# Optimization experiments

Hardware: AMD Instinct MI355X
Metric: run time of the kernel (lower is better)

## Reference

```python
import jax, jax.numpy as jnp
import numpy as np
from jax import lax
from jax.scipy.special import logsumexp

KX = jnp.array([[1., 0., -1.], [2., 0., -2.], [1., 0., -1.]], jnp.float32).reshape(1, 1, 3, 3)
KY = jnp.array([[1., 2., 1.], [0., 0., 0.], [-1., -2., -1.]], jnp.float32).reshape(1, 1, 3, 3)
SINK_EPS = 0.05 ** 2  # geomloss SamplesLoss('sinkhorn', p=2, blur=0.05): eps = blur**p
SINK_ITERS = 10
N_SUB = 4096


def _gauss1d(size, sigma):
    x = jnp.arange(size, dtype=jnp.float32) - (size - 1) / 2.0
    k = jnp.exp(-(x * x) / (2.0 * sigma * sigma))
    return k / k.sum()


def _sep_filter(x, k, sym_pad):
    # separable 2D filter; x [B,C,H,W], k [ks]. VALID conv; optional symmetric pad (scipy 'reflect').
    B, C, H, W = x.shape
    xr = x.reshape(B * C, 1, H, W)
    if sym_pad:
        r = k.shape[0] // 2
        xr = jnp.pad(xr, ((0, 0), (0, 0), (r, r), (r, r)), mode='symmetric')
    o = lax.conv_general_dilated(xr, k.reshape(1, 1, -1, 1), (1, 1), 'VALID')
    o = lax.conv_general_dilated(o, k.reshape(1, 1, 1, -1), (1, 1), 'VALID')
    return o.reshape(B, C, o.shape[2], o.shape[3])


def _ssim_per_sample(x, y):
    # standard gaussian-window SSIM (11x11, sigma=1.5, data_range=1.0), mean per sample -> [B]
    k = _gauss1d(11, 1.5)
    mu1, mu2 = _sep_filter(x, k, False), _sep_filter(y, k, False)
    s11 = _sep_filter(x * x, k, False) - mu1 * mu1
    s22 = _sep_filter(y * y, k, False) - mu2 * mu2
    s12 = _sep_filter(x * y, k, False) - mu1 * mu2
    C1, C2 = 0.01 ** 2, 0.03 ** 2
    m = ((2 * mu1 * mu2 + C1) * (2 * s12 + C2)) / ((mu1 * mu1 + mu2 * mu2 + C1) * (s11 + s22 + C2))
    return m.mean(axis=(1, 2, 3))


def _sobel(x):
    # SobelGrad.forward: per-channel magnitude, per-(b,c) max-normalized, channel-mean -> [B,1,H,W]
    B, C, H, W = x.shape
    xr = x.reshape(B * C, 1, H, W)
    gx = lax.conv_general_dilated(xr, KX, (1, 1), ((1, 1), (1, 1)))
    gy = lax.conv_general_dilated(xr, KY, (1, 1), ((1, 1), (1, 1)))
    mag = jnp.sqrt(gx * gx + gy * gy + 1e-6).reshape(B, C, H, W)
    mag = mag / jnp.maximum(mag.max(axis=(2, 3), keepdims=True), 1e-6)
    return mag.mean(1, keepdims=True)


def _avgpool2(x):
    B, C, H, W = x.shape
    return x.reshape(B, C, H // 2, 2, W // 2, 2).mean(axis=(3, 5))


def _charb_mean(d):
    return jnp.sqrt(d * d + 1e-6).mean()  # charbonnier eps=1e-3


def _ot_eps(x, y):
    # entropic OT value with uniform weights, log-domain Sinkhorn, envelope gradient (geomloss-style:
    # iterations detached, one differentiable update at the end).
    N, M = x.shape[0], y.shape[0]
    C = 0.5 * (jnp.sum(x * x, 1)[:, None] + jnp.sum(y * y, 1)[None, :] - 2.0 * x @ y.T)  # p=2 cost |x-y|^2/2
    Cd = lax.stop_gradient(C)
    loga, logb = -float(np.log(N)), -float(np.log(M))
    def body(carry, _):
        f, g = carry
        g = -SINK_EPS * logsumexp(loga + (f[:, None] - Cd) / SINK_EPS, axis=0)
        f = -SINK_EPS * logsumexp(logb + (g[None, :] - Cd) / SINK_EPS, axis=1)
        return (f, g), None
    (f, g), _ = lax.scan(body, (jnp.zeros((N,), x.dtype), jnp.zeros((M,), x.dtype)), None, length=SINK_ITERS)
    f = lax.stop_gradient(f)
    g = -SINK_EPS * logsumexp(loga + (f[:, None] - C) / SINK_EPS, axis=0)
    f = -SINK_EPS * logsumexp(logb + (g[None, :] - C) / SINK_EPS, axis=1)
    return f.mean() + g.mean()


def _sinkhorn_div(x, y):
    return _ot_eps(x, y) - 0.5 * _ot_eps(x, x) - 0.5 * _ot_eps(y, y)


def _forward(y, mri, pet, mask, ehat, idx):
    B, C, H, W = y.shape
    y_gray = y.mean(1, keepdims=True)
    ssim_m = 1.0 - _ssim_per_sample(y_gray, mri).mean()
    ssim_p = 1.0 - _ssim_per_sample(y, pet).mean()
    g_cons = (_charb_mean(_sobel(y_gray) - _sobel(mri))
              + _charb_mean(_sobel(_avgpool2(y).mean(1, keepdims=True)) - _sobel(_avgpool2(mri))))
    aux = jnp.abs(ehat - lax.stop_gradient(_sobel(mri))).mean()
    # per-sample masked point clouds, fixed 4096-point subsample (idx ~ randperm[:4096])
    y_pts = (y * mask).reshape(B, C, H * W).transpose(0, 2, 1)    # [B,HW,3]
    pet_pts = (pet * mask).reshape(B, C, H * W).transpose(0, 2, 1)
    y_s = jnp.take_along_axis(y_pts, idx[..., None], axis=1)      # [B,4096,3]
    pet_s = jnp.take_along_axis(pet_pts, idx[..., None], axis=1)
    include = ((mask.reshape(B, -1) > 0.1).sum(1) >= 32).astype(y.dtype)  # 'continue' guard
    L_transport = (include * jax.vmap(_sinkhorn_div)(y_s, pet_s)).sum() / B
    L_out = (include * ((y * (1.0 - mask)) ** 2).mean(axis=(1, 2, 3))).sum() / B
    mri_rgb = jnp.broadcast_to(mri, y.shape)
    L_ssim = (include * (1.0 - _ssim_per_sample(y * mask, mri_rgb * mask))).sum() / B
    loss_transport = 0.8 * L_transport + 0.3 * L_out + 0.5 * L_ssim  # alpha, beta, gamma
    L_intensity = 2.5 * jnp.mean((y * mask - pet * mask) ** 2)
    # gaussian_smooth: scipy gaussian_filter sigma=1, truncate=4 -> radius 4, mode 'reflect';
    # torch path detaches before smoothing -> stop_gradient
    smoothed = lax.stop_gradient(_sep_filter(y, _gauss1d(9, 1.0), True))
    L_smooth = jnp.mean((smoothed - y) ** 2)
    total = loss_transport + L_intensity + 0.2 * L_smooth
    return total, ssim_m, ssim_p, g_cons, aux


def setup_inputs() -> dict:
    key = jax.random.key(0)
    ks = jax.random.split(key, 5)
    B, C, H, W = 2, 3, 256, 256
    y = jax.random.uniform(ks[0], (B, C, H, W), jnp.float32)
    mri = jax.random.uniform(ks[1], (B, 1, H, W), jnp.float32)
    pet = jax.random.uniform(ks[2], (B, C, H, W), jnp.float32)
    mask = jax.random.uniform(ks[3], (B, 1, H, W), jnp.float32)
    ehat = jax.random.uniform(ks[4], (B, 1, H, W), jnp.float32)
    rng = np.random.default_rng(0)
    idx = jnp.asarray(np.stack([rng.permutation(H * W)[:N_SUB] for _ in range(B)]), dtype=jnp.int32)
    return {"y": y, "mri": mri, "pet": pet, "mask": mask, "ehat": ehat, "idx": idx}


def reference(y, mri, pet, mask, ehat, idx):
    return _forward(y, mri, pet, mask, ehat, idx)
```

## Files before the change

### kernel.cpp

```cpp
#include <hip/hip_runtime.h>
#include <math.h>

#define INV_EPS_L2E 577.0780163555854f
#define EPS_LOGN 0.02079441542f
#define EPS_LN2 0.00173286795f

#define NPTS 4096
#define CHUNK 64
#define NCH 64
#define CPT 8
#define COLS_PER_BLK 2048
#define NCB 2
#define QSTRIDE (NCH * NPTS)

typedef float v2f __attribute__((ext_vector_type(2)));

constexpr int A_SSIMA  = 0;
constexpr int A_SSIMB  = 2;
constexpr int A_SSIMC  = 4;
constexpr int A_CH1    = 6;
constexpr int A_CH2    = 7;
constexpr int A_AUX    = 8;
constexpr int A_INT    = 9;
constexpr int A_LOUT   = 10;
constexpr int A_CNT    = 12;
constexpr int A_SMOOTH = 14;
constexpr int A_SINK   = 16;
constexpr int A_MAX    = 32;

__device__ __forceinline__ float blockSum(float v, int tid) {
#pragma unroll
    for (int o = 32; o; o >>= 1) v += __shfl_down(v, o, 64);
    __shared__ float sh[4];
    __syncthreads();
    if ((tid & 63) == 0) sh[tid >> 6] = v;
    __syncthreads();
    return sh[0] + sh[1] + sh[2] + sh[3];
}

__device__ __forceinline__ float blockMax(float v, int tid) {
#pragma unroll
    for (int o = 32; o; o >>= 1) v = fmaxf(v, __shfl_down(v, o, 64));
    __shared__ float sh[4];
    __syncthreads();
    if ((tid & 63) == 0) sh[tid >> 6] = v;
    __syncthreads();
    return fmaxf(fmaxf(sh[0], sh[1]), fmaxf(sh[2], sh[3]));
}

__global__ __launch_bounds__(256) void egf_prep(const float* __restrict__ y,
                                                const float* __restrict__ pet,
                                                const float* __restrict__ mask,
                                                float* __restrict__ ygray,
                                                float* __restrict__ acc) {
    int b = blockIdx.y;
    int p = blockIdx.x * 256 + threadIdx.x;
    float m  = mask[b * 65536 + p];
    float y0 = y[(b * 3 + 0) * 65536 + p];
    float y1 = y[(b * 3 + 1) * 65536 + p];
    float y2 = y[(b * 3 + 2) * 65536 + p];
    float q0 = pet[(b * 3 + 0) * 65536 + p];
    float q1 = pet[(b * 3 + 1) * 65536 + p];
    float q2 = pet[(b * 3 + 2) * 65536 + p];
    ygray[b * 65536 + p] = (y0 + y1 + y2) * (1.0f / 3.0f);
    float d0 = m * y0 - m * q0, d1 = m * y1 - m * q1, d2 = m * y2 - m * q2;
    float inten = d0 * d0 + d1 * d1 + d2 * d2;
    float im = 1.0f - m;
    float o0 = y0 * im, o1 = y1 * im, o2 = y2 * im;
    float lout = o0 * o0 + o1 * o1 + o2 * o2;
    float cnt = (m > 0.1f) ? 1.0f : 0.0f;
    float t;
    t = blockSum(inten, threadIdx.x); if (threadIdx.x == 0) atomicAdd(&acc[A_INT], t);
    t = blockSum(lout,  threadIdx.x); if (threadIdx.x == 0) atomicAdd(&acc[A_LOUT + b], t);
    t = blockSum(cnt,   threadIdx.x); if (threadIdx.x == 0) atomicAdd(&acc[A_CNT + b], t);
}

__global__ __launch_bounds__(256) void egf_pool(const float* __restrict__ y,
                                                const float* __restrict__ mri,
                                                float* __restrict__ py,
                                                float* __restrict__ pmri) {
    int b = blockIdx.y;
    int po = blockIdx.x * 256 + threadIdx.x;
    int i = po >> 7, j = po & 127;
    int p0 = (i * 2) * 256 + j * 2;
    float s = 0.0f;
#pragma unroll
    for (int c = 0; c < 3; c++) {
        const float* ip = y + (b * 3 + c) * 65536;
        s += ip[p0] + ip[p0 + 1] + ip[p0 + 256] + ip[p0 + 257];
    }
    py[b * 16384 + po] = s * (1.0f / 12.0f);
    const float* mp = mri + b * 65536;
    pmri[b * 16384 + po] = (mp[p0] + mp[p0 + 1] + mp[p0 + 256] + mp[p0 + 257]) * 0.25f;
}

__global__ __launch_bounds__(256) void egf_sobel(const float* __restrict__ in,
                                                 float* __restrict__ mag,
                                                 unsigned* __restrict__ mx,
                                                 int H, int logH) {
    int b = blockIdx.y;
    int p = blockIdx.x * 256 + threadIdx.x;
    int HH = H * H;
    const float* ip = in + b * HH;
    int i = p >> logH, j = p & (H - 1);
    auto at = [&](int ii, int jj) -> float {
        return (ii >= 0 && ii < H && jj >= 0 && jj < H) ? ip[(ii << logH) + jj] : 0.0f;
    };
    float a00 = at(i - 1, j - 1), a01 = at(i - 1, j), a02 = at(i - 1, j + 1);
    float a10 = at(i, j - 1),                         a12 = at(i, j + 1);
    float a20 = at(i + 1, j - 1), a21 = at(i + 1, j), a22 = at(i + 1, j + 1);
    float gx = a00 - a02 + 2.0f * a10 - 2.0f * a12 + a20 - a22;
    float gy = a00 + 2.0f * a01 + a02 - a20 - 2.0f * a21 - a22;
    float m = sqrtf(gx * gx + gy * gy + 1e-6f);
    mag[b * HH + p] = m;
    float bm = blockMax(m, threadIdx.x);
    if (threadIdx.x == 0) atomicMax(mx + b, __float_as_uint(bm));
}

__global__ __launch_bounds__(256) void egf_charb(const float* __restrict__ magA,
                                                 const float* __restrict__ magB,
                                                 const unsigned* __restrict__ mxA,
                                                 const unsigned* __restrict__ mxB,
                                                 const float* __restrict__ ehat,
                                                 float* __restrict__ accC,
                                                 float* __restrict__ accAux,
                                                 int HH) {
    int b = blockIdx.y;
    int p = blockIdx.x * 256 + threadIdx.x;
    float c = 0.0f, au = 0.0f;
    float da = fmaxf(__uint_as_float(mxA[b]), 1e-6f);
    float db = fmaxf(__uint_as_float(mxB[b]), 1e-6f);
    if (p < HH) {
        float sa = magA[b * HH + p] / da;
        float sb = magB[b * HH + p] / db;
        float d = sa - sb;
        c = sqrtf(d * d + 1e-6f);
        if (ehat) au = fabsf(ehat[b * HH + p] - sb);
    }
    float tc = blockSum(c, threadIdx.x);
    if (threadIdx.x == 0) atomicAdd(accC, tc);
    if (ehat) {
        float ta = blockSum(au, threadIdx.x);
        if (threadIdx.x == 0) atomicAdd(accAux, ta);
    }
}

__global__ __launch_bounds__(256) void egf_ssim(const float* __restrict__ X, int xBS, int xCS,
                                                const float* __restrict__ Y, int yBS, int yCS,
                                                const float* __restrict__ M,
                                                int C_, float* __restrict__ accB) {
    int bc = blockIdx.z; int b = bc / C_; int c = bc - b * C_;
    const float* xp = X + b * xBS + c * xCS;
    const float* yp = Y + b * yBS + c * yCS;
    const float* mp = M ? (M + b * 65536) : nullptr;
    __shared__ float sx[26][27];
    __shared__ float sy[26][27];
    int ti = blockIdx.x * 16, tj = blockIdx.y * 16;
    int tid = threadIdx.y * 16 + threadIdx.x;
    for (int t = tid; t < 26 * 26; t += 256) {
        int li = t / 26, lj = t - li * 26;
        int gi = ti + li, gj = tj + lj;
        float a = 0.0f, bb = 0.0f;
        if (gi < 256 && gj < 256) {
            int p = (gi << 8) + gj;
            float m = mp ? mp[p] : 1.0f;
            a = xp[p] * m; bb = yp[p] * m;
        }
        sx[li][lj] = a; sy[li][lj] = bb;
    }
    __syncthreads();
    float w[11];
    {
        float s = 0.0f;
#pragma unroll
        for (int i = 0; i < 11; i++) { float d = (float)(i - 5); w[i] = expf(-d * d * (1.0f / 4.5f)); s += w[i]; }
        float inv = 1.0f / s;
#pragma unroll
        for (int i = 0; i < 11; i++) w[i] *= inv;
    }
    int oi = ti + threadIdx.y, oj = tj + threadIdx.x;
    float val = 0.0f;
    if (oi < 246 && oj < 246) {
        float mu1 = 0, mu2 = 0, xx = 0, yy = 0, xy = 0;
        for (int di = 0; di < 11; di++) {
            float wi = w[di];
#pragma unroll
            for (int dj = 0; dj < 11; dj++) {
                float ww = wi * w[dj];
                float a  = sx[threadIdx.y + di][threadIdx.x + dj];
                float bb = sy[threadIdx.y + di][threadIdx.x + dj];
                mu1 += ww * a; mu2 += ww * bb;
                xx += ww * a * a; yy += ww * bb * bb; xy += ww * a * bb;
            }
        }
        float s11 = xx - mu1 * mu1, s22 = yy - mu2 * mu2, s12 = xy - mu1 * mu2;
        const float C1 = 1e-4f, C2 = 9e-4f;
        val = ((2.0f * mu1 * mu2 + C1) * (2.0f * s12 + C2)) /
              ((mu1 * mu1 + mu2 * mu2 + C1) * (s11 + s22 + C2));
    }
    float tot = blockSum(val, tid);
    if (tid == 0) atomicAdd(&accB[b], tot);
}

__device__ __forceinline__ int refl256(int i) { return i < 0 ? -1 - i : (i > 255 ? 511 - i : i); }

__device__ __forceinline__ void gauss9(float* w) {
    float s = 0.0f;
#pragma unroll
    for (int t = 0; t < 9; t++) { float d = (float)(t - 4); w[t] = expf(-0.5f * d * d); s += w[t]; }
    float inv = 1.0f / s;
#pragma unroll
    for (int t = 0; t < 9; t++) w[t] *= inv;
}

__global__ __launch_bounds__(256) void egf_smoothV(const float* __restrict__ y, float* __restrict__ tmp) {
    int g = blockIdx.x * 256 + threadIdx.x;
    int bc = g >> 16; int p = g & 65535; int i = p >> 8, j = p & 255;
    float w[9]; gauss9(w);
    const float* ip = y + bc * 65536;
    float s = 0.0f;
#pragma unroll
    for (int t = 0; t < 9; t++) s += w[t] * ip[(refl256(i + t - 4) << 8) + j];
    tmp[g] = s;
}

__global__ __launch_bounds__(256) void egf_smoothH(const float* __restrict__ tmp,
                                                   const float* __restrict__ y,
                                                   float* __restrict__ acc) {
    int g = blockIdx.x * 256 + threadIdx.x;
    int bc = g >> 16; int p = g & 65535; int i = p >> 8, j = p & 255;
    float w[9]; gauss9(w);
    const float* tp = tmp + bc * 65536;
    float s = 0.0f;
#pragma unroll
    for (int t = 0; t < 9; t++) s += w[t] * tp[(i << 8) + refl256(j + t - 4)];
    float d = s - y[g];
    float tt = blockSum(d * d, threadIdx.x);
    if (threadIdx.x == 0) atomicAdd(acc, tt);
}

__global__ __launch_bounds__(256) void egf_gather(const float* __restrict__ y,
                                                  const float* __restrict__ pet,
                                                  const float* __restrict__ mask,
                                                  const int* __restrict__ idx,
                                                  float4* __restrict__ pts) {
    int t = blockIdx.x * 256 + threadIdx.x;
    int b = t >> 12, j = t & 4095;
    int p = idx[b * 4096 + j];
    float m = mask[b * 65536 + p];
    float a0 = y[(b * 3 + 0) * 65536 + p] * m;
    float a1 = y[(b * 3 + 1) * 65536 + p] * m;
    float a2 = y[(b * 3 + 2) * 65536 + p] * m;
    pts[(b * 2 + 0) * 4096 + j] = make_float4(a0, a1, a2, 0.5f * (a0 * a0 + a1 * a1 + a2 * a2));
    float c0 = pet[(b * 3 + 0) * 65536 + p] * m;
    float c1 = pet[(b * 3 + 1) * 65536 + p] * m;
    float c2 = pet[(b * 3 + 2) * 65536 + p] * m;
    pts[(b * 2 + 1) * 4096 + j] = make_float4(c0, c1, c2, 0.5f * (c0 * c0 + c1 * c1 + c2 * c2));
}

__device__ __forceinline__ float stageCombine(const float* __restrict__ Pin_m,
                                              const float* __restrict__ Pin_s,
                                              int qbase, int row, int h, int r_local,
                                              float* sm, float* ss, int tid) {
    const float* pm = Pin_m + qbase + h * 16 * NPTS + row;
    const float* ps = Pin_s + qbase + h * 16 * NPTS + row;
    float mv[16], sv[16];
#pragma unroll
    for (int k = 0; k < 16; k++) mv[k] = pm[k * NPTS];
#pragma unroll
    for (int k = 0; k < 16; k++) sv[k] = ps[k * NPTS];
    float m16 = -3.4e38f;
#pragma unroll
    for (int k = 0; k < 16; k++) m16 = fmaxf(m16, mv[k]);
    float s16 = 0.0f;
#pragma unroll
    for (int k = 0; k < 16; k++) s16 += sv[k] * __builtin_amdgcn_exp2f(mv[k] - m16);
    sm[h * 64 + r_local] = m16;
    ss[h * 64 + r_local] = s16;
    __syncthreads();
    float v = 0.0f;
    if (tid < 64) {
        float m0 = sm[tid], m1 = sm[64 + tid], m2 = sm[128 + tid], m3 = sm[192 + tid];
        float M = fmaxf(fmaxf(m0, m1), fmaxf(m2, m3));
        float S = ss[tid]       * __builtin_amdgcn_exp2f(m0 - M) +
                  ss[64 + tid]  * __builtin_amdgcn_exp2f(m1 - M) +
                  ss[128 + tid] * __builtin_amdgcn_exp2f(m2 - M) +
                  ss[192 + tid] * __builtin_amdgcn_exp2f(m3 - M);
        v = EPS_LOGN - EPS_LN2 * (M + log2f(S));
    }
    return v;
}

__global__ __launch_bounds__(256) void egf_sink_half5(const float4* __restrict__ pts,
                                                      const float* __restrict__ Pin_m,
                                                      const float* __restrict__ Pin_s,
                                                      float* __restrict__ Pout_m,
                                                      float* __restrict__ Pout_s,
                                                      int dir, int init) {
    int q = blockIdx.z; int b = q / 3, t = q - b * 3;
    int xsel = (t == 2) ? 1 : 0;
    int ysel = (t == 1) ? 0 : 1;
    int rsel = (dir == 0) ? xsel : ysel;
    int csel = (dir == 0) ? ysel : xsel;
    const float4* rowP = pts + (b * 2 + rsel) * NPTS;
    const float4* colP = pts + (b * 2 + csel) * NPTS;

    __shared__ float4 srow[CHUNK];
    __shared__ float sm[256], ss[256];
    int tid = threadIdx.x;
    int chunk = blockIdx.y;
    int r_local = tid & 63, h = tid >> 6;
    int row = chunk * CHUNK + r_local;

    float v = 0.0f;
    if (!init)
        v = stageCombine(Pin_m, Pin_s, q * QSTRIDE, row, h, r_local, sm, ss, tid);
    if (tid < 64) {
        float4 pp = rowP[row];
        srow[tid] = make_float4(pp.x * INV_EPS_L2E, pp.y * INV_EPS_L2E,
                                pp.z * INV_EPS_L2E, (v - pp.w) * INV_EPS_L2E);
    }
    __syncthreads();

    int col0 = blockIdx.x * COLS_PER_BLK + tid;
    v2f cx[4], cy[4], cz[4], cw[4];
#pragma unroll
    for (int p = 0; p < 4; p++) {
        float4 c0 = colP[col0 + (2 * p) * 256];
        float4 c1 = colP[col0 + (2 * p + 1) * 256];
        cx[p] = (v2f){c0.x, c1.x};
        cy[p] = (v2f){c0.y, c1.y};
        cz[p] = (v2f){c0.z, c1.z};
        cw[p] = (v2f){c0.w * INV_EPS_L2E, c1.w * INV_EPS_L2E};
    }
    v2f mx[4];
#pragma unroll
    for (int p = 0; p < 4; p++) mx[p] = -3.4e38f;
#pragma unroll 4
    for (int r = 0; r < CHUNK; r++) {
        float4 rp = srow[r];
        v2f rx = rp.x, ry = rp.y, rz = rp.z, rw = rp.w;
#pragma unroll
        for (int p = 0; p < 4; p++) {
            v2f e = rw;
            e = __builtin_elementwise_fma(rx, cx[p], e);
            e = __builtin_elementwise_fma(ry, cy[p], e);
            e = __builtin_elementwise_fma(rz, cz[p], e);
            mx[p] = __builtin_elementwise_max(mx[p], e);
        }
    }
    v2f sa[4];
#pragma unroll
    for (int p = 0; p < 4; p++) sa[p] = 0.0f;
#pragma unroll 4
    for (int r = 0; r < CHUNK; r++) {
        float4 rp = srow[r];
        v2f rx = rp.x, ry = rp.y, rz = rp.z, rw = rp.w;
#pragma unroll
        for (int p = 0; p < 4; p++) {
            v2f e = rw - mx[p];
            e = __builtin_elementwise_fma(rx, cx[p], e);
            e = __builtin_elementwise_fma(ry, cy[p], e);
            e = __builtin_elementwise_fma(rz, cz[p], e);
            v2f ex;
            ex.x = __builtin_amdgcn_exp2f(e.x);
            ex.y = __builtin_amdgcn_exp2f(e.y);
            sa[p] += ex;
        }
    }
    float* om = Pout_m + q * QSTRIDE + chunk * NPTS;
    float* os = Pout_s + q * QSTRIDE + chunk * NPTS;
#pragma unroll
    for (int p = 0; p < 4; p++) {
        v2f mstore = mx[p] - cw[p];
        om[col0 + (2 * p) * 256]     = mstore.x;
        om[col0 + (2 * p + 1) * 256] = mstore.y;
        os[col0 + (2 * p) * 256]     = sa[p].x;
        os[col0 + (2 * p + 1) * 256] = sa[p].y;
    }
}

__global__ __launch_bounds__(256) void egf_sink_val5(const float* __restrict__ Pf_m,
                                                     const float* __restrict__ Pf_s,
                                                     const float* __restrict__ Pg_m,
                                                     const float* __restrict__ Pg_s,
                                                     float* __restrict__ acc) {
    int q = blockIdx.y;
    int side = blockIdx.x >> 6;
    int chunk = blockIdx.x & 63;
    const float* Pm = side ? Pg_m : Pf_m;
    const float* Ps = side ? Pg_s : Pf_s;
    __shared__ float sm[256], ss[256];
    int tid = threadIdx.x;
    int r_local = tid & 63, h = tid >> 6;
    int row = chunk * CHUNK + r_local;
    float v = stageCombine(Pm, Ps, q * QSTRIDE, row, h, r_local, sm, ss, tid);
    float tot = blockSum(v, tid);
    if (tid == 0) atomicAdd(&acc[A_SINK + q], tot * (1.0f / 4096.0f));
}

__global__ void egf_finalize(const float* __restrict__ acc, float* __restrict__ out) {
    if (threadIdx.x != 0 || blockIdx.x != 0) return;
    const float AREA = 246.0f * 246.0f;
    float ssim_m = 1.0f - (acc[A_SSIMA] + acc[A_SSIMA + 1]) / (2.0f * AREA);
    float ssim_p = 1.0f - (acc[A_SSIMB] + acc[A_SSIMB + 1]) / (2.0f * 3.0f * AREA);
    float g_cons = acc[A_CH1] / (2.0f * 65536.0f) + acc[A_CH2] / (2.0f * 16384.0f);
    float aux = acc[A_AUX] / (2.0f * 65536.0f);
    float inc0 = (acc[A_CNT]     >= 31.5f) ? 1.0f : 0.0f;
    float inc1 = (acc[A_CNT + 1] >= 31.5f) ? 1.0f : 0.0f;
    const float* v = acc + A_SINK;
    float Lt = (inc0 * (v[0] - 0.5f * v[1] - 0.5f * v[2]) +
                inc1 * (v[3] - 0.5f * v[4] - 0.5f * v[5])) * 0.5f;
    float Lo = (inc0 * acc[A_LOUT] + inc1 * acc[A_LOUT + 1]) / (3.0f * 65536.0f) * 0.5f;
    float Ls = (inc0 * (1.0f - acc[A_SSIMC] / (3.0f * AREA)) +
                inc1 * (1.0f - acc[A_SSIMC + 1] / (3.0f * AREA))) * 0.5f;
    float Li = 2.5f * acc[A_INT] / (2.0f * 3.0f * 65536.0f);
    float Lsm = acc[A_SMOOTH] / (2.0f * 3.0f * 65536.0f);
    float total = 0.8f * Lt + 0.3f * Lo + 0.5f * Ls + Li + 0.2f * Lsm;
    out[0] = total; out[1] = ssim_m; out[2] = ssim_p; out[3] = g_cons; out[4] = aux;
}

extern "C" void kernel_launch(void* const* d_in, const int* in_sizes, int n_in,
                              void* d_out, int out_size, void* d_ws, size_t ws_size,
                              hipStream_t stream) {
    const float* y    = (const float*)d_in[0];
    const float* mri  = (const float*)d_in[1];
    const float* pet  = (const float*)d_in[2];
    const float* mask = (const float*)d_in[3];
    const float* ehat = (const float*)d_in[4];
    const int*   idx  = (const int*)d_in[5];
    float* out = (float*)d_out;
    float* ws  = (float*)d_ws;

    float* acc   = ws;
    float4* pts  = (float4*)(ws + 64);
    float* base  = ws + 64 + 65536;

    float* Pf_m = base;
    float* Pf_s = base + QSTRIDE * 6;
    float* Pg_m = base + 2 * QSTRIDE * 6;
    float* Pg_s = base + 3 * QSTRIDE * 6;
    float* ibase = base + 4 * QSTRIDE * 6;

    float* ygray    = ibase;
    float* py       = ygray + 131072;
    float* pmri     = py + 32768;
    float* mag_yg   = pmri + 32768;
    float* mag_mri  = mag_yg + 131072;
    float* mag_py   = mag_mri + 131072;
    float* mag_pmri = mag_py + 32768;
    float* tmp      = mag_pmri + 32768;

    hipMemsetAsync(acc, 0, 64 * sizeof(float), stream);

    unsigned* mx = (unsigned*)(acc + A_MAX);

    egf_prep<<<dim3(256, 2), 256, 0, stream>>>(y, pet, mask, ygray, acc);
    egf_pool<<<dim3(64, 2), 256, 0, stream>>>(y, mri, py, pmri);
    egf_sobel<<<dim3(256, 2), 256, 0, stream>>>(ygray, mag_yg, mx + 0, 256, 8);
    egf_sobel<<<dim3(256, 2), 256, 0, stream>>>(mri, mag_mri, mx + 2, 256, 8);
    egf_sobel<<<dim3(64, 2), 256, 0, stream>>>(py, mag_py, mx + 4, 128, 7);
    egf_sobel<<<dim3(64, 2), 256, 0, stream>>>(pmri, mag_pmri, mx + 6, 128, 7);
    egf_charb<<<dim3(256, 2), 256, 0, stream>>>(mag_yg, mag_mri, mx + 0, mx + 2, ehat,
                                                acc + A_CH1, acc + A_AUX, 65536);
    egf_charb<<<dim3(64, 2), 256, 0, stream>>>(mag_py, mag_pmri, mx + 4, mx + 6, nullptr,
                                               acc + A_CH2, nullptr, 16384);
    egf_ssim<<<dim3(16, 16, 2), dim3(16, 16), 0, stream>>>(ygray, 65536, 0, mri, 65536, 0,
                                                           nullptr, 1, acc + A_SSIMA);
    egf_ssim<<<dim3(16, 16, 6), dim3(16, 16), 0, stream>>>(y, 196608, 65536, pet, 196608, 65536,
                                                           nullptr, 3, acc + A_SSIMB);
    egf_ssim<<<dim3(16, 16, 6), dim3(16, 16), 0, stream>>>(y, 196608, 65536, mri, 65536, 0,
                                                           mask, 3, acc + A_SSIMC);
    egf_smoothV<<<1536, 256, 0, stream>>>(y, tmp);
    egf_smoothH<<<1536, 256, 0, stream>>>(tmp, y, acc + A_SMOOTH);
    egf_gather<<<32, 256, 0, stream>>>(y, pet, mask, idx, pts);

    dim3 sgrid(NCB, NCH, 6);
    for (int it = 0; it < 11; ++it) {
        egf_sink_half5<<<sgrid, 256, 0, stream>>>(pts, Pf_m, Pf_s, Pg_m, Pg_s, 0, it == 0 ? 1 : 0);
        egf_sink_half5<<<sgrid, 256, 0, stream>>>(pts, Pg_m, Pg_s, Pf_m, Pf_s, 1, 0);
    }
    egf_sink_val5<<<dim3(128, 6), 256, 0, stream>>>(Pf_m, Pf_s, Pg_m, Pg_s, acc);
    egf_finalize<<<1, 64, 0, stream>>>(acc, out);
}
```

Before: 874.0 us.

## Fuse Sinkhorn half-iterations into one persistent cooperative kernel with grid sync

Replaces the 22 separate Sinkhorn half-step launches with a single cooperative persistent kernel. Blocks loop over the 768 tiles and use grid-wide syncs between half-iterations. The aim is to remove per-launch overhead and the drain/refill gaps between the small kernels. In exchange, grid.sync adds its own cost, and if the grid is smaller than the tile count some blocks process tiles serially. A fallback to the old launch loop runs if the cooperative launch fails.

New measurement: 2.066 ms. 2.36x slower.

```diff
diff --git a/kernel.cpp b/kernel.cpp
--- a/kernel.cpp
+++ b/kernel.cpp
@@ -1,5 +1,8 @@
 #include <hip/hip_runtime.h>
+#include <hip/hip_cooperative_groups.h>
 #include <math.h>
+
+namespace cg = cooperative_groups;
 
 #define INV_EPS_L2E 577.0780163555854f
 #define EPS_LOGN 0.02079441542f
@@ -11,6 +14,7 @@
 #define CPT 8
 #define COLS_PER_BLK 2048
 #define NCB 2
+#define NTILES 768
 #define QSTRIDE (NCH * NPTS)
 
 typedef float v2f __attribute__((ext_vector_type(2)));
@@ -291,26 +295,25 @@
     return v;
 }
 
-__global__ __launch_bounds__(256) void egf_sink_half5(const float4* __restrict__ pts,
-                                                      const float* __restrict__ Pin_m,
-                                                      const float* __restrict__ Pin_s,
-                                                      float* __restrict__ Pout_m,
-                                                      float* __restrict__ Pout_s,
-                                                      int dir, int init) {
-    int q = blockIdx.z; int b = q / 3, t = q - b * 3;
+__device__ __forceinline__ void sinkTileBody(const float4* __restrict__ pts,
+                                             const float* __restrict__ Pin_m,
+                                             const float* __restrict__ Pin_s,
+                                             float* __restrict__ Pout_m,
+                                             float* __restrict__ Pout_s,
+                                             int dir, int init, int tile,
+                                             float4* srow, float* sm, float* ss, int tid) {
+    int q = tile >> 7;
+    int r = tile & 127;
+    int chunk = r >> 1;
+    int cb = r & 1;
+    int b = q / 3, t = q - b * 3;
     int xsel = (t == 2) ? 1 : 0;
     int ysel = (t == 1) ? 0 : 1;
-    int rsel = (dir == 0) ? xsel : ysel;
-    int csel = (dir == 0) ? ysel : xsel;
-    const float4* rowP = pts + (b * 2 + rsel) * NPTS;
-    const float4* colP = pts + (b * 2 + csel) * NPTS;
-
-    __shared__ float4 srow[CHUNK];
-    __shared__ float sm[256], ss[256];
-    int tid = threadIdx.x;
-    int chunk = blockIdx.y;
+    const float4* rowP = pts + (b * 2 + (dir ? ysel : xsel)) * NPTS;
+    const float4* colP = pts + (b * 2 + (dir ? xsel : ysel)) * NPTS;
     int r_local = tid & 63, h = tid >> 6;
     int row = chunk * CHUNK + r_local;
+    int col0 = cb * COLS_PER_BLK + tid;
 
     float v = 0.0f;
     if (!init)
@@ -322,7 +325,6 @@
     }
     __syncthreads();
 
-    int col0 = blockIdx.x * COLS_PER_BLK + tid;
     v2f cx[4], cy[4], cz[4], cw[4];
 #pragma unroll
     for (int p = 0; p < 4; p++) {
@@ -337,8 +339,8 @@
 #pragma unroll
     for (int p = 0; p < 4; p++) mx[p] = -3.4e38f;
 #pragma unroll 4
-    for (int r = 0; r < CHUNK; r++) {
-        float4 rp = srow[r];
+    for (int rr = 0; rr < CHUNK; rr++) {
+        float4 rp = srow[rr];
         v2f rx = rp.x, ry = rp.y, rz = rp.z, rw = rp.w;
 #pragma unroll
         for (int p = 0; p < 4; p++) {
@@ -353,8 +355,8 @@
 #pragma unroll
     for (int p = 0; p < 4; p++) sa[p] = 0.0f;
 #pragma unroll 4
-    for (int r = 0; r < CHUNK; r++) {
-        float4 rp = srow[r];
+    for (int rr = 0; rr < CHUNK; rr++) {
+        float4 rp = srow[rr];
         v2f rx = rp.x, ry = rp.y, rz = rp.z, rw = rp.w;
 #pragma unroll
         for (int p = 0; p < 4; p++) {
@@ -378,6 +380,45 @@
         os[col0 + (2 * p) * 256]     = sa[p].x;
         os[col0 + (2 * p + 1) * 256] = sa[p].y;
     }
+    __syncthreads();
+}
+
+__global__ __launch_bounds__(256, 3) void egf_sink_coop(const float4* __restrict__ pts,
+                                                        float* __restrict__ Pf_m,
+                                                        float* __restrict__ Pf_s,
+                                                        float* __restrict__ Pg_m,
+                                                        float* __restrict__ Pg_s,
+                                                        int ntiles) {
+    cg::grid_group grid = cg::this_grid();
+    __shared__ float4 srow[CHUNK];
+    __shared__ float sm[256], ss[256];
+    int tid = threadIdx.x;
+    int nb = gridDim.x;
+
+    for (int hh = 0; hh < 22; hh++) {
+        int dir = hh & 1;
+        const float* Pin_m = dir ? Pg_m : Pf_m;
+        const float* Pin_s = dir ? Pg_s : Pf_s;
+        float* Pout_m = dir ? Pf_m : Pg_m;
+        float* Pout_s = dir ? Pf_s : Pg_s;
+        for (int tile = blockIdx.x; tile < ntiles; tile += nb)
+            sinkTileBody(pts, Pin_m, Pin_s, Pout_m, Pout_s, dir, hh == 0, tile,
+                         srow, sm, ss, tid);
+        if (hh < 21) grid.sync();
+    }
+}
+
+__global__ __launch_bounds__(256) void egf_sink_half5(const float4* __restrict__ pts,
+                                                      const float* __restrict__ Pin_m,
+                                                      const float* __restrict__ Pin_s,
+                                                      float* __restrict__ Pout_m,
+                                                      float* __restrict__ Pout_s,
+                                                      int dir, int init) {
+    __shared__ float4 srow[CHUNK];
+    __shared__ float sm[256], ss[256];
+    int tile = blockIdx.z * 128 + blockIdx.y * 2 + blockIdx.x;
+    sinkTileBody(pts, Pin_m, Pin_s, Pout_m, Pout_s, dir, init, tile,
+                 srow, sm, ss, (int)threadIdx.x);
 }
 
 __global__ __launch_bounds__(256) void egf_sink_val5(const float* __restrict__ Pf_m,
@@ -475,10 +516,30 @@
     egf_smoothH<<<1536, 256, 0, stream>>>(tmp, y, acc + A_SMOOTH);
     egf_gather<<<32, 256, 0, stream>>>(y, pet, mask, idx, pts);
 
-    dim3 sgrid(NCB, NCH, 6);
-    for (int it = 0; it < 11; ++it) {
-        egf_sink_half5<<<sgrid, 256, 0, stream>>>(pts, Pf_m, Pf_s, Pg_m, Pg_s, 0, it == 0 ? 1 : 0);
-        egf_sink_half5<<<sgrid, 256, 0, stream>>>(pts, Pg_m, Pg_s, Pf_m, Pf_s, 1, 0);
+    bool coop_done = false;
+    {
+        int perCU = 0, numCU = 0, dev = 0;
+        hipGetDevice(&dev);
+        hipDeviceGetAttribute(&numCU, hipDeviceAttributeMultiprocessorCount, dev);
+        hipError_t oe = hipOccupancyMaxActiveBlocksPerMultiprocessor(&perCU, egf_sink_coop, 256, 0);
+        int maxBlocks = (oe == hipSuccess) ? perCU * numCU : 0;
+        int grid = maxBlocks < NTILES ? maxBlocks : NTILES;
+        if (grid > 0) {
+            const float4* pts_c = (const float4*)pts;
+            int ntiles = NTILES;
+            void* args[] = {(void*)&pts_c, (void*)&Pf_m, (void*)&Pf_s,
+                            (void*)&Pg_m, (void*)&Pg_s, (void*)&ntiles};
+            hipError_t le = hipLaunchCooperativeKernel((void*)egf_sink_coop, dim3(grid),
+                                                       dim3(256), args, 0, stream);
+            coop_done = (le == hipSuccess);
+        }
+    }
+    if (!coop_done) {
+        dim3 sgrid(NCB, NCH, 6);
+        for (int it = 0; it < 11; ++it) {
+            egf_sink_half5<<<sgrid, 256, 0, stream>>>(pts, Pf_m, Pf_s, Pg_m, Pg_s, 0, it == 0 ? 1 : 0);
+            egf_sink_half5<<<sgrid, 256, 0, stream>>>(pts, Pg_m, Pg_s, Pf_m, Pf_s, 1, 0);
+        }
     }
     egf_sink_val5<<<dim3(128, 6), 256, 0, stream>>>(Pf_m, Pf_s, Pg_m, Pg_s, acc);
     egf_finalize<<<1, 64, 0, stream>>>(acc, out);
```

## Interleave Sinkhorn partial max/sum into float2 and halve row chunk size

Applied to the files above, without the earlier changes.

Sinkhorn partial results are now stored as interleaved (max, sum) float2 pairs instead of two separate arrays, so each partial needs one wider load and one wider store. The row chunk shrinks from 64 to 32, doubling the number of chunks and blocks to 128 per side, and the combine stage now merges 8 groups of 16 partials. Launch bounds request 6 blocks per CU. In exchange there are twice as many partial-result columns to write and read each half-iteration, which raises memory traffic.

Result: slower. 963.5 us (+10.2%).

```diff
diff --git a/kernel.cpp b/kernel.cpp
--- a/kernel.cpp
+++ b/kernel.cpp
@@ -6,8 +6,8 @@
 #define EPS_LN2 0.00173286795f
 
 #define NPTS 4096
-#define CHUNK 64
-#define NCH 64
+#define CHUNK 32
+#define NCH 128
 #define CPT 8
 #define COLS_PER_BLK 2048
 #define NCB 2
@@ -258,64 +258,58 @@
     pts[(b * 2 + 1) * 4096 + j] = make_float4(c0, c1, c2, 0.5f * (c0 * c0 + c1 * c1 + c2 * c2));
 }
 
-__device__ __forceinline__ float stageCombine(const float* __restrict__ Pin_m,
-                                              const float* __restrict__ Pin_s,
-                                              int qbase, int row, int h, int r_local,
+__device__ __forceinline__ float stageCombine(const float2* __restrict__ Pin,
+                                              int qbase, int row, int h,
                                               float* sm, float* ss, int tid) {
-    const float* pm = Pin_m + qbase + h * 16 * NPTS + row;
-    const float* ps = Pin_s + qbase + h * 16 * NPTS + row;
-    float mv[16], sv[16];
-#pragma unroll
-    for (int k = 0; k < 16; k++) mv[k] = pm[k * NPTS];
-#pragma unroll
-    for (int k = 0; k < 16; k++) sv[k] = ps[k * NPTS];
+    const float2* p = Pin + qbase + (h * 16) * NPTS + row;
+    float2 t[16];
+#pragma unroll
+    for (int k = 0; k < 16; k++) t[k] = p[k * NPTS];
     float m16 = -3.4e38f;
 #pragma unroll
-    for (int k = 0; k < 16; k++) m16 = fmaxf(m16, mv[k]);
+    for (int k = 0; k < 16; k++) m16 = fmaxf(m16, t[k].x);
     float s16 = 0.0f;
 #pragma unroll
-    for (int k = 0; k < 16; k++) s16 += sv[k] * __builtin_amdgcn_exp2f(mv[k] - m16);
-    sm[h * 64 + r_local] = m16;
-    ss[h * 64 + r_local] = s16;
+    for (int k = 0; k < 16; k++) s16 += t[k].y * __builtin_amdgcn_exp2f(t[k].x - m16);
+    sm[tid] = m16;
+    ss[tid] = s16;
     __syncthreads();
     float v = 0.0f;
-    if (tid < 64) {
-        float m0 = sm[tid], m1 = sm[64 + tid], m2 = sm[128 + tid], m3 = sm[192 + tid];
-        float M = fmaxf(fmaxf(m0, m1), fmaxf(m2, m3));
-        float S = ss[tid]       * __builtin_amdgcn_exp2f(m0 - M) +
-                  ss[64 + tid]  * __builtin_amdgcn_exp2f(m1 - M) +
-                  ss[128 + tid] * __builtin_amdgcn_exp2f(m2 - M) +
-                  ss[192 + tid] * __builtin_amdgcn_exp2f(m3 - M);
+    if (tid < 32) {
+        float M = -3.4e38f;
+        float mj[8];
+#pragma unroll
+        for (int j = 0; j < 8; j++) { mj[j] = sm[j * 32 + tid]; M = fmaxf(M, mj[j]); }
+        float S = 0.0f;
+#pragma unroll
+        for (int j = 0; j < 8; j++)
+            S += ss[j * 32 + tid] * __builtin_amdgcn_exp2f(mj[j] - M);
         v = EPS_LOGN - EPS_LN2 * (M + log2f(S));
     }
     return v;
 }
 
-__global__ __launch_bounds__(256) void egf_sink_half5(const float4* __restrict__ pts,
-                                                      const float* __restrict__ Pin_m,
-                                                      const float* __restrict__ Pin_s,
-                                                      float* __restrict__ Pout_m,
-                                                      float* __restrict__ Pout_s,
-                                                      int dir, int init) {
+__global__ __launch_bounds__(256, 6) void egf_sink_half6(const float4* __restrict__ pts,
+                                                         const float2* __restrict__ Pin,
+                                                         float2* __restrict__ Pout,
+                                                         int dir, int init) {
     int q = blockIdx.z; int b = q / 3, t = q - b * 3;
     int xsel = (t == 2) ? 1 : 0;
     int ysel = (t == 1) ? 0 : 1;
-    int rsel = (dir == 0) ? xsel : ysel;
-    int csel = (dir == 0) ? ysel : xsel;
-    const float4* rowP = pts + (b * 2 + rsel) * NPTS;
-    const float4* colP = pts + (b * 2 + csel) * NPTS;
+    const float4* rowP = pts + (b * 2 + (dir ? ysel : xsel)) * NPTS;
+    const float4* colP = pts + (b * 2 + (dir ? xsel : ysel)) * NPTS;
 
     __shared__ float4 srow[CHUNK];
     __shared__ float sm[256], ss[256];
     int tid = threadIdx.x;
     int chunk = blockIdx.y;
-    int r_local = tid & 63, h = tid >> 6;
+    int r_local = tid & 31, h = tid >> 5;
     int row = chunk * CHUNK + r_local;
 
     float v = 0.0f;
     if (!init)
-        v = stageCombine(Pin_m, Pin_s, q * QSTRIDE, row, h, r_local, sm, ss, tid);
-    if (tid < 64) {
+        v = stageCombine(Pin, q * QSTRIDE, row, h, sm, ss, tid);
+    if (tid < 32) {
         float4 pp = rowP[row];
         srow[tid] = make_float4(pp.x * INV_EPS_L2E, pp.y * INV_EPS_L2E,
                                 pp.z * INV_EPS_L2E, (v - pp.w) * INV_EPS_L2E);
@@ -337,8 +331,8 @@
 #pragma unroll
     for (int p = 0; p < 4; p++) mx[p] = -3.4e38f;
 #pragma unroll 4
-    for (int r = 0; r < CHUNK; r++) {
-        float4 rp = srow[r];
+    for (int rr = 0; rr < CHUNK; rr++) {
+        float4 rp = srow[rr];
         v2f rx = rp.x, ry = rp.y, rz = rp.z, rw = rp.w;
 #pragma unroll
         for (int p = 0; p < 4; p++) {
@@ -353,8 +347,8 @@
 #pragma unroll
     for (int p = 0; p < 4; p++) sa[p] = 0.0f;
 #pragma unroll 4
-    for (int r = 0; r < CHUNK; r++) {
-        float4 rp = srow[r];
+    for (int rr = 0; rr < CHUNK; rr++) {
+        float4 rp = srow[rr];
         v2f rx = rp.x, ry = rp.y, rz = rp.z, rw = rp.w;
 #pragma unroll
         for (int p = 0; p < 4; p++) {
@@ -368,33 +362,27 @@
             sa[p] += ex;
         }
     }
-    float* om = Pout_m + q * QSTRIDE + chunk * NPTS;
-    float* os = Pout_s + q * QSTRIDE + chunk * NPTS;
+    float2* om = Pout + q * QSTRIDE + chunk * NPTS;
 #pragma unroll
     for (int p = 0; p < 4; p++) {
         v2f mstore = mx[p] - cw[p];
-        om[col0 + (2 * p) * 256]     = mstore.x;
-        om[col0 + (2 * p + 1) * 256] = mstore.y;
-        os[col0 + (2 * p) * 256]     = sa[p].x;
-        os[col0 + (2 * p + 1) * 256] = sa[p].y;
-    }
-}
-
-__global__ __launch_bounds__(256) void egf_sink_val5(const float* __restrict__ Pf_m,
-                                                     const float* __restrict__ Pf_s,
-                                                     const float* __restrict__ Pg_m,
-                                                     const float* __restrict__ Pg_s,
+        om[col0 + (2 * p) * 256]     = make_float2(mstore.x, sa[p].x);
+        om[col0 + (2 * p + 1) * 256] = make_float2(mstore.y, sa[p].y);
+    }
+}
+
+__global__ __launch_bounds__(256) void egf_sink_val6(const float2* __restrict__ Pf,
+                                                     const float2* __restrict__ Pg,
                                                      float* __restrict__ acc) {
     int q = blockIdx.y;
-    int side = blockIdx.x >> 6;
-    int chunk = blockIdx.x & 63;
-    const float* Pm = side ? Pg_m : Pf_m;
-    const float* Ps = side ? Pg_s : Pf_s;
+    int side = blockIdx.x >> 7;
+    int chunk = blockIdx.x & 127;
+    const float2* P = side ? Pg : Pf;
     __shared__ float sm[256], ss[256];
     int tid = threadIdx.x;
-    int r_local = tid & 63, h = tid >> 6;
+    int r_local = tid & 31, h = tid >> 5;
     int row = chunk * CHUNK + r_local;
-    float v = stageCombine(Pm, Ps, q * QSTRIDE, row, h, r_local, sm, ss, tid);
+    float v = stageCombine(P, q * QSTRIDE, row, h, sm, ss, tid);
     float tot = blockSum(v, tid);
     if (tid == 0) atomicAdd(&acc[A_SINK + q], tot * (1.0f / 4096.0f));
 }
@@ -436,10 +424,8 @@
     float4* pts  = (float4*)(ws + 64);
     float* base  = ws + 64 + 65536;
 
-    float* Pf_m = base;
-    float* Pf_s = base + QSTRIDE * 6;
-    float* Pg_m = base + 2 * QSTRIDE * 6;
-    float* Pg_s = base + 3 * QSTRIDE * 6;
+    float2* Pf = (float2*)base;
+    float2* Pg = Pf + QSTRIDE * 6;
     float* ibase = base + 4 * QSTRIDE * 6;
 
     float* ygray    = ibase;
@@ -477,9 +463,9 @@
 
     dim3 sgrid(NCB, NCH, 6);
     for (int it = 0; it < 11; ++it) {
-        egf_sink_half5<<<sgrid, 256, 0, stream>>>(pts, Pf_m, Pf_s, Pg_m, Pg_s, 0, it == 0 ? 1 : 0);
-        egf_sink_half5<<<sgrid, 256, 0, stream>>>(pts, Pg_m, Pg_s, Pf_m, Pf_s, 1, 0);
-    }
-    egf_sink_val5<<<dim3(128, 6), 256, 0, stream>>>(Pf_m, Pf_s, Pg_m, Pg_s, acc);
+        egf_sink_half6<<<sgrid, 256, 0, stream>>>(pts, Pf, Pg, 0, it == 0 ? 1 : 0);
+        egf_sink_half6<<<sgrid, 256, 0, stream>>>(pts, Pg, Pf, 1, 0);
+    }
+    egf_sink_val6<<<dim3(256, 6), 256, 0, stream>>>(Pf, Pg, acc);
     egf_finalize<<<1, 64, 0, stream>>>(acc, out);
 }
```
